# Kernel optimization log

Measured on AMD Instinct MI355X. Metric: run time of the kernel, lower is better.

## Reference

```python
import jax, jax.numpy as jnp
import numpy as np

B, T, D = 2, 2048, 1024
F = 4096
E = 8


def setup_inputs() -> dict:
    key = jax.random.key(0)
    k0, k1, k2, k3 = jax.random.split(key, 4)
    x = jax.random.normal(k0, (B, T, D), dtype=jnp.float32)
    Wg = jax.random.normal(k1, (E, D), dtype=jnp.float32) * 0.02   # gate Linear weight [E, D]
    W1 = jax.random.normal(k2, (E, D, F), dtype=jnp.float32) * 0.02  # expert up-proj
    W2 = jax.random.normal(k3, (E, F, D), dtype=jnp.float32) * 0.02  # expert down-proj
    return {"x": x, "Wg": Wg, "W1": W1, "W2": W2}


def reference(x, Wg, W1, W2):
    b, t, d = x.shape
    h = x.reshape(-1, d)                              # [N, D], N = b*t
    # --- top-2 gate ---
    logits = h @ Wg.T                                 # [N, E]
    scores, idx = jax.lax.top_k(logits, 2)            # [N, 2], [N, 2]
    scores = jax.nn.softmax(scores.astype(jnp.float32), axis=-1).astype(x.dtype)
    # --- all-expert dense FFN (SiLU MLP) ---
    up = jnp.einsum('nd,edf->enf', h, W1)             # [E, N, F]
    act = jax.nn.silu(up)
    out = jnp.einsum('enf,efd->ned', act, W2)         # [N, E, D]
    # --- combine top-2 ---
    sel = jnp.take_along_axis(out, idx[:, :, None], axis=1)  # [N, 2, D]
    y = jnp.sum(scores[:, :, None] * sel, axis=1)     # [N, D]
    return y.reshape(b, t, d)
```

## Files before the change

kernel.cpp:

```cpp
#include <hip/hip_runtime.h>
#include <hip/hip_bf16.h>
#include <stdint.h>

#define N_TOK 4096
#define D_DIM 1024
#define F_DIM 4096
#define E_NUM 8

typedef unsigned short u16;
typedef __attribute__((ext_vector_type(8))) short short8;
typedef __attribute__((ext_vector_type(4))) float f32x4;

__device__ __forceinline__ u16 f2bf(float f) {
  union { float f; uint32_t u; } v; v.f = f;
  uint32_t u = v.u;
  uint32_t r = (u + 0x7FFFu + ((u >> 16) & 1u)) >> 16;
  return (u16)r;
}

__device__ __forceinline__ void gld_lds16(const u16* g, u16* l) {
  __builtin_amdgcn_global_load_lds(
      (const __attribute__((address_space(1))) uint32_t*)g,
      (__attribute__((address_space(3))) uint32_t*)l, 16, 0, 0);
}

__global__ __launch_bounds__(256) void transpose_cvt_kernel(
    const float* __restrict__ in, u16* __restrict__ out, int R, int C) {
  __shared__ u16 tile[64][72];
  int e = blockIdx.z;
  int r0 = blockIdx.y * 64, c0 = blockIdx.x * 64;
  const float* src = in + (size_t)e * R * C;
  u16* dst = out + (size_t)e * R * C;
  int tid = threadIdx.x;
  int lr = tid & 15;
  int rr = tid >> 4;
#pragma unroll
  for (int p = 0; p < 4; ++p) {
    int r = rr + p * 16;
    float4 v = *(const float4*)&src[(size_t)(r0 + r) * C + c0 + lr * 4];
    tile[lr * 4 + 0][r] = f2bf(v.x);
    tile[lr * 4 + 1][r] = f2bf(v.y);
    tile[lr * 4 + 2][r] = f2bf(v.z);
    tile[lr * 4 + 3][r] = f2bf(v.w);
  }
  __syncthreads();
#pragma unroll
  for (int p = 0; p < 4; ++p) {
    int c = rr + p * 16;
    ushort4 o = *(const ushort4*)&tile[c][lr * 4];
    *(ushort4*)&dst[(size_t)(c0 + c) * R + r0 + lr * 4] = o;
  }
}

__global__ void gate_kernel(const float* __restrict__ x, const float* __restrict__ Wg,
                            u16* __restrict__ xb, int2* __restrict__ choice,
                            float* __restrict__ sc2) {
  int n = blockIdx.x;
  int l = threadIdx.x;
  const float* xr = x + (size_t)n * D_DIM;
  u16* xbr = xb + (size_t)n * D_DIM;
  float acc[E_NUM];
#pragma unroll
  for (int e = 0; e < E_NUM; ++e) acc[e] = 0.f;
  for (int d = l; d < D_DIM; d += 64) {
    float xv = xr[d];
    xbr[d] = f2bf(xv);
#pragma unroll
    for (int e = 0; e < E_NUM; ++e) acc[e] += xv * Wg[e * D_DIM + d];
  }
#pragma unroll
  for (int e = 0; e < E_NUM; ++e) {
    float v = acc[e];
#pragma unroll
    for (int off = 32; off > 0; off >>= 1) v += __shfl_xor(v, off);
    acc[e] = v;
  }
  if (l == 0) {
    int i0 = 0; float m0 = acc[0];
#pragma unroll
    for (int e = 1; e < E_NUM; ++e) if (acc[e] > m0) { m0 = acc[e]; i0 = e; }
    int i1 = -1; float m1 = -INFINITY;
#pragma unroll
    for (int e = 0; e < E_NUM; ++e) if (e != i0 && acc[e] > m1) { m1 = acc[e]; i1 = e; }
    float z = expf(m1 - m0);
    float s0 = 1.f / (1.f + z);
    sc2[n * 2 + 0] = s0;
    sc2[n * 2 + 1] = 1.f - s0;
    choice[n] = make_int2(i0, i1);
  }
}

__global__ void route_kernel(const int2* __restrict__ choice, int* __restrict__ cnt,
                             int* __restrict__ tok_list) {
  int e = blockIdx.x;
  int l = threadIdx.x;
  unsigned long long below = (l == 0) ? 0ull : ((~0ull) >> (64 - l));
  int c = 0;
  for (int it = 0; it < N_TOK / 64; ++it) {
    int n = it * 64 + l;
    int2 ch = choice[n];
    unsigned long long b0 = __ballot(ch.x == e);
    if (ch.x == e) tok_list[e * N_TOK + c + __popcll(b0 & below)] = 2 * n;
    c += __popcll(b0);
    unsigned long long b1 = __ballot(ch.y == e);
    if (ch.y == e) tok_list[e * N_TOK + c + __popcll(b1 & below)] = 2 * n + 1;
    c += __popcll(b1);
  }
  if (l == 0) cnt[e] = c;
}

__global__ void prefix_kernel(const int* __restrict__ cnt, int* __restrict__ base) {
  if (threadIdx.x == 0) {
    int s = 0;
    for (int e = 0; e < E_NUM; ++e) { base[e] = s; s += cnt[e]; }
  }
}


__global__ __launch_bounds__(256) void up_gemm(
    const u16* __restrict__ xb, const u16* __restrict__ w1t,
    const int* __restrict__ cnt, const int* __restrict__ base,
    const int* __restrict__ tok_list, u16* __restrict__ act) {
  __shared__ u16 As[128 * 32];
  __shared__ u16 Bs[128 * 32];

  const int e = blockIdx.z;
  const int ce = cnt[e];
  const int row0 = blockIdx.y * 128;
  if (row0 >= ce) return;
  const int col0 = blockIdx.x * 128;
  const int be = base[e];

  const int tid = threadIdx.x;
  const int wave = tid >> 6, lane = tid & 63;
  const int wm = wave >> 1, wn = wave & 1;
  const int lr = lane & 15, kq = lane >> 4;

  const int rs0 = wave * 32 + (lane >> 2);
  const int rs1 = rs0 + 16;
  const int kb = (((lane & 3) ^ ((lane >> 3) & 3)) * 8);
  const int kq8 = ((kq ^ ((lr >> 1) & 3)) * 8);

  int ga0 = row0 + rs0, ga1 = row0 + rs1;
  int e0 = (ga0 < ce) ? (tok_list[e * N_TOK + ga0] & (2 * N_TOK - 1)) : 0;
  int e1 = (ga1 < ce) ? (tok_list[e * N_TOK + ga1] & (2 * N_TOK - 1)) : 0;
  const u16* srcA0 = xb + (e0 >> 1) * D_DIM + kb;
  const u16* srcA1 = xb + (e1 >> 1) * D_DIM + kb;
  const u16* srcB0 = w1t + (size_t)(e * F_DIM + col0 + rs0) * D_DIM + kb;
  const u16* srcB1 = w1t + (size_t)(e * F_DIM + col0 + rs1) * D_DIM + kb;
  u16* ldsA0 = As + (wave * 2 + 0) * 512;
  u16* ldsA1 = As + (wave * 2 + 1) * 512;
  u16* ldsB0 = Bs + (wave * 2 + 0) * 512;
  u16* ldsB1 = Bs + (wave * 2 + 1) * 512;

  f32x4 acc[4][4];
#pragma unroll
  for (int m = 0; m < 4; ++m)
#pragma unroll
    for (int n = 0; n < 4; ++n) acc[m][n] = (f32x4){0.f, 0.f, 0.f, 0.f};

  for (int k0 = 0; k0 < D_DIM; k0 += 32) {
    gld_lds16(srcA0 + k0, ldsA0);
    gld_lds16(srcA1 + k0, ldsA1);
    gld_lds16(srcB0 + k0, ldsB0);
    gld_lds16(srcB1 + k0, ldsB1);
    __syncthreads();
    short8 a[4], b[4];
#pragma unroll
    for (int m = 0; m < 4; ++m)
      a[m] = *(const short8*)&As[(wm * 64 + m * 16 + lr) * 32 + kq8];
#pragma unroll
    for (int n = 0; n < 4; ++n)
      b[n] = *(const short8*)&Bs[(wn * 64 + n * 16 + lr) * 32 + kq8];
#pragma unroll
    for (int m = 0; m < 4; ++m)
#pragma unroll
      for (int n = 0; n < 4; ++n)
        acc[m][n] = __builtin_amdgcn_mfma_f32_16x16x32_bf16(a[m], b[n], acc[m][n], 0, 0, 0);
    __syncthreads();
  }

#pragma unroll
  for (int m = 0; m < 4; ++m) {
#pragma unroll
    for (int rg = 0; rg < 4; ++rg) {
      int row = wm * 64 + m * 16 + kq * 4 + rg;
      int i = row0 + row;
      if (i < ce) {
        u16* dst = act + (size_t)(be + i) * F_DIM + col0 + wn * 64;
#pragma unroll
        for (int n = 0; n < 4; ++n) {
          float v = acc[m][n][rg];
          float s = v / (1.f + expf(-v));
          dst[n * 16 + lr] = f2bf(s);
        }
      }
    }
  }
}

__global__ __launch_bounds__(256) void down_gemm(
    const u16* __restrict__ act, const u16* __restrict__ w2t,
    const int* __restrict__ cnt, const int* __restrict__ base,
    const int* __restrict__ tok_list, const float* __restrict__ sc2,
    float* __restrict__ out) {
  __shared__ u16 As[128 * 32];
  __shared__ u16 Bs[128 * 32];
  __shared__ int toks[128];

  const int e = blockIdx.z;
  const int ce = cnt[e];
  const int row0 = blockIdx.y * 128;
  if (row0 >= ce) return;
  const int col0 = blockIdx.x * 128;
  const int be = base[e];

  const int tid = threadIdx.x;
  const int wave = tid >> 6, lane = tid & 63;
  const int wm = wave >> 1, wn = wave & 1;
  const int lr = lane & 15, kq = lane >> 4;

  if (tid < 128) {
    int i = row0 + tid;
    toks[tid] = (i < ce) ? tok_list[e * N_TOK + i] : -1;
  }

  const int rs0 = wave * 32 + (lane >> 2);
  const int rs1 = rs0 + 16;
  const int kb = (((lane & 3) ^ ((lane >> 3) & 3)) * 8);
  const int kq8 = ((kq ^ ((lr >> 1) & 3)) * 8);

  int ra0 = min(be + row0 + rs0, 2 * N_TOK - 1);
  int ra1 = min(be + row0 + rs1, 2 * N_TOK - 1);
  const u16* srcA0 = act + (size_t)ra0 * F_DIM + kb;
  const u16* srcA1 = act + (size_t)ra1 * F_DIM + kb;
  const u16* srcB0 = w2t + (size_t)(e * D_DIM + col0 + rs0) * F_DIM + kb;
  const u16* srcB1 = w2t + (size_t)(e * D_DIM + col0 + rs1) * F_DIM + kb;
  u16* ldsA0 = As + (wave * 2 + 0) * 512;
  u16* ldsA1 = As + (wave * 2 + 1) * 512;
  u16* ldsB0 = Bs + (wave * 2 + 0) * 512;
  u16* ldsB1 = Bs + (wave * 2 + 1) * 512;

  f32x4 acc[4][4];
#pragma unroll
  for (int m = 0; m < 4; ++m)
#pragma unroll
    for (int n = 0; n < 4; ++n) acc[m][n] = (f32x4){0.f, 0.f, 0.f, 0.f};

  for (int k0 = 0; k0 < F_DIM; k0 += 32) {
    gld_lds16(srcA0 + k0, ldsA0);
    gld_lds16(srcA1 + k0, ldsA1);
    gld_lds16(srcB0 + k0, ldsB0);
    gld_lds16(srcB1 + k0, ldsB1);
    __syncthreads();
    short8 a[4], b[4];
#pragma unroll
    for (int m = 0; m < 4; ++m)
      a[m] = *(const short8*)&As[(wm * 64 + m * 16 + lr) * 32 + kq8];
#pragma unroll
    for (int n = 0; n < 4; ++n)
      b[n] = *(const short8*)&Bs[(wn * 64 + n * 16 + lr) * 32 + kq8];
#pragma unroll
    for (int m = 0; m < 4; ++m)
#pragma unroll
      for (int n = 0; n < 4; ++n)
        acc[m][n] = __builtin_amdgcn_mfma_f32_16x16x32_bf16(a[m], b[n], acc[m][n], 0, 0, 0);
    __syncthreads();
  }

#pragma unroll
  for (int m = 0; m < 4; ++m) {
#pragma unroll
    for (int rg = 0; rg < 4; ++rg) {
      int row = wm * 64 + m * 16 + kq * 4 + rg;
      int ent = toks[row];
      if (ent >= 0) {
        int tokn = ent >> 1;
        float sc = sc2[tokn * 2 + (ent & 1)];
        float* dst = out + (size_t)tokn * D_DIM + col0 + wn * 64;
#pragma unroll
        for (int n = 0; n < 4; ++n)
          atomicAdd(&dst[n * 16 + lr], acc[m][n][rg] * sc);
      }
    }
  }
}

extern "C" void kernel_launch(void* const* d_in, const int* in_sizes, int n_in,
                              void* d_out, int out_size, void* d_ws, size_t ws_size,
                              hipStream_t stream) {
  const float* x  = (const float*)d_in[0];
  const float* Wg = (const float*)d_in[1];
  const float* W1 = (const float*)d_in[2];
  const float* W2 = (const float*)d_in[3];
  float* out = (float*)d_out;

  char* ws = (char*)d_ws;
  size_t off = 0;
  u16* xb  = (u16*)(ws + off); off += (size_t)N_TOK * D_DIM * 2;
  u16* w1t = (u16*)(ws + off); off += (size_t)E_NUM * F_DIM * D_DIM * 2;
  u16* w2t = (u16*)(ws + off); off += (size_t)E_NUM * D_DIM * F_DIM * 2;
  u16* act = (u16*)(ws + off); off += (size_t)2 * N_TOK * F_DIM * 2;
  int* tok_list = (int*)(ws + off); off += (size_t)E_NUM * N_TOK * 4;
  float* sc2 = (float*)(ws + off); off += (size_t)N_TOK * 2 * 4;
  int2* choice = (int2*)(ws + off); off += (size_t)N_TOK * 8;
  int* cnt  = (int*)(ws + off); off += 128;
  int* base = (int*)(ws + off); off += 128;

  hipMemsetAsync(d_out, 0, (size_t)out_size * 4, stream);

  {
    dim3 blk(256, 1, 1);
    dim3 g1(F_DIM / 64, D_DIM / 64, E_NUM);
    transpose_cvt_kernel<<<g1, blk, 0, stream>>>(W1, w1t, D_DIM, F_DIM);
    dim3 g2(D_DIM / 64, F_DIM / 64, E_NUM);
    transpose_cvt_kernel<<<g2, blk, 0, stream>>>(W2, w2t, F_DIM, D_DIM);
  }

  gate_kernel<<<N_TOK, 64, 0, stream>>>(x, Wg, xb, choice, sc2);
  route_kernel<<<E_NUM, 64, 0, stream>>>(choice, cnt, tok_list);
  prefix_kernel<<<1, 1, 0, stream>>>(cnt, base);

  {
    dim3 g(F_DIM / 128, N_TOK / 128, E_NUM);
    up_gemm<<<g, 256, 0, stream>>>(xb, w1t, cnt, base, tok_list, act);
  }
  {
    dim3 g(D_DIM / 128, N_TOK / 128, E_NUM);
    down_gemm<<<g, 256, 0, stream>>>(act, w2t, cnt, base, tok_list, sc2, out);
  }
}
```

Before: 374.0 us.

## Remap GEMM blocks to XCD-local experts and widen down_gemm to eight waves

Both expert GEMMs now launch a flat 1D grid whose block index is permuted so every block dispatched to a given XCD (round-robin by block id) works on the same expert, aiming to keep that expert's weights resident in the XCD-local L2. The down projection also moves from 4 to 8 waves per block with a 2x4 wave layout and 64x32 per-wave tiles, to raise occupancy and latency hiding. The trade-off is fewer MFMAs per LDS read per wave and more threads sharing each barrier.

```diff
diff --git a/kernel.cpp b/kernel.cpp
--- a/kernel.cpp
+++ b/kernel.cpp
@@ -124,11 +124,14 @@
   __shared__ u16 As[128 * 32];
   __shared__ u16 Bs[128 * 32];
 
-  const int e = blockIdx.z;
+  const int bid = blockIdx.x;
+  const int orig = (bid & 7) * 1024 + (bid >> 3);
+  const int bx = orig & 31, by = (orig >> 5) & 31, e = orig >> 10;
+
   const int ce = cnt[e];
-  const int row0 = blockIdx.y * 128;
+  const int row0 = by * 128;
   if (row0 >= ce) return;
-  const int col0 = blockIdx.x * 128;
+  const int col0 = bx * 128;
   const int be = base[e];
 
   const int tid = threadIdx.x;
@@ -199,7 +202,7 @@
   }
 }
 
-__global__ __launch_bounds__(256) void down_gemm(
+__global__ __launch_bounds__(512) void down_gemm(
     const u16* __restrict__ act, const u16* __restrict__ w2t,
     const int* __restrict__ cnt, const int* __restrict__ base,
     const int* __restrict__ tok_list, const float* __restrict__ sc2,
@@ -208,16 +211,19 @@
   __shared__ u16 Bs[128 * 32];
   __shared__ int toks[128];
 
-  const int e = blockIdx.z;
+  const int bid = blockIdx.x;
+  const int orig = (bid & 7) * 256 + (bid >> 3);
+  const int bx = orig & 7, by = (orig >> 3) & 31, e = orig >> 8;
+
   const int ce = cnt[e];
-  const int row0 = blockIdx.y * 128;
+  const int row0 = by * 128;
   if (row0 >= ce) return;
-  const int col0 = blockIdx.x * 128;
+  const int col0 = bx * 128;
   const int be = base[e];
 
   const int tid = threadIdx.x;
   const int wave = tid >> 6, lane = tid & 63;
-  const int wm = wave >> 1, wn = wave & 1;
+  const int wm = wave >> 2, wn = wave & 3;
   const int lr = lane & 15, kq = lane >> 4;
 
   if (tid < 128) {
@@ -225,45 +231,37 @@
     toks[tid] = (i < ce) ? tok_list[e * N_TOK + i] : -1;
   }
 
-  const int rs0 = wave * 32 + (lane >> 2);
-  const int rs1 = rs0 + 16;
+  const int rsA = wave * 16 + (lane >> 2);
   const int kb = (((lane & 3) ^ ((lane >> 3) & 3)) * 8);
   const int kq8 = ((kq ^ ((lr >> 1) & 3)) * 8);
 
-  int ra0 = min(be + row0 + rs0, 2 * N_TOK - 1);
-  int ra1 = min(be + row0 + rs1, 2 * N_TOK - 1);
-  const u16* srcA0 = act + (size_t)ra0 * F_DIM + kb;
-  const u16* srcA1 = act + (size_t)ra1 * F_DIM + kb;
-  const u16* srcB0 = w2t + (size_t)(e * D_DIM + col0 + rs0) * F_DIM + kb;
-  const u16* srcB1 = w2t + (size_t)(e * D_DIM + col0 + rs1) * F_DIM + kb;
-  u16* ldsA0 = As + (wave * 2 + 0) * 512;
-  u16* ldsA1 = As + (wave * 2 + 1) * 512;
-  u16* ldsB0 = Bs + (wave * 2 + 0) * 512;
-  u16* ldsB1 = Bs + (wave * 2 + 1) * 512;
-
-  f32x4 acc[4][4];
+  int ra = min(be + row0 + rsA, 2 * N_TOK - 1);
+  const u16* srcA = act + (size_t)ra * F_DIM + kb;
+  const u16* srcB = w2t + (size_t)(e * D_DIM + col0 + rsA) * F_DIM + kb;
+  u16* ldsA = As + wave * 512;
+  u16* ldsB = Bs + wave * 512;
+
+  f32x4 acc[4][2];
 #pragma unroll
   for (int m = 0; m < 4; ++m)
 #pragma unroll
-    for (int n = 0; n < 4; ++n) acc[m][n] = (f32x4){0.f, 0.f, 0.f, 0.f};
+    for (int n = 0; n < 2; ++n) acc[m][n] = (f32x4){0.f, 0.f, 0.f, 0.f};
 
   for (int k0 = 0; k0 < F_DIM; k0 += 32) {
-    gld_lds16(srcA0 + k0, ldsA0);
-    gld_lds16(srcA1 + k0, ldsA1);
-    gld_lds16(srcB0 + k0, ldsB0);
-    gld_lds16(srcB1 + k0, ldsB1);
+    gld_lds16(srcA + k0, ldsA);
+    gld_lds16(srcB + k0, ldsB);
     __syncthreads();
-    short8 a[4], b[4];
+    short8 a[4], b[2];
 #pragma unroll
     for (int m = 0; m < 4; ++m)
       a[m] = *(const short8*)&As[(wm * 64 + m * 16 + lr) * 32 + kq8];
 #pragma unroll
-    for (int n = 0; n < 4; ++n)
-      b[n] = *(const short8*)&Bs[(wn * 64 + n * 16 + lr) * 32 + kq8];
+    for (int n = 0; n < 2; ++n)
+      b[n] = *(const short8*)&Bs[(wn * 32 + n * 16 + lr) * 32 + kq8];
 #pragma unroll
     for (int m = 0; m < 4; ++m)
 #pragma unroll
-      for (int n = 0; n < 4; ++n)
+      for (int n = 0; n < 2; ++n)
         acc[m][n] = __builtin_amdgcn_mfma_f32_16x16x32_bf16(a[m], b[n], acc[m][n], 0, 0, 0);
     __syncthreads();
   }
@@ -277,9 +275,9 @@
       if (ent >= 0) {
         int tokn = ent >> 1;
         float sc = sc2[tokn * 2 + (ent & 1)];
-        float* dst = out + (size_t)tokn * D_DIM + col0 + wn * 64;
-#pragma unroll
-        for (int n = 0; n < 4; ++n)
+        float* dst = out + (size_t)tokn * D_DIM + col0 + wn * 32;
+#pragma unroll
+        for (int n = 0; n < 2; ++n)
           atomicAdd(&dst[n * 16 + lr], acc[m][n][rg] * sc);
       }
     }
@@ -321,12 +319,6 @@
   route_kernel<<<E_NUM, 64, 0, stream>>>(choice, cnt, tok_list);
   prefix_kernel<<<1, 1, 0, stream>>>(cnt, base);
 
-  {
-    dim3 g(F_DIM / 128, N_TOK / 128, E_NUM);
-    up_gemm<<<g, 256, 0, stream>>>(xb, w1t, cnt, base, tok_list, act);
-  }
-  {
-    dim3 g(D_DIM / 128, N_TOK / 128, E_NUM);
-    down_gemm<<<g, 256, 0, stream>>>(act, w2t, cnt, base, tok_list, sc2, out);
-  }
-}
+  up_gemm<<<dim3(8192), 256, 0, stream>>>(xb, w1t, cnt, base, tok_list, act);
+  down_gemm<<<dim3(2048), 512, 0, stream>>>(act, w2t, cnt, base, tok_list, sc2, out);
+}
```

Result: faster. 336.9 us (-9.9%).
